# Performance work log

Measured on AMD Instinct MI355X. Metric: run time of the kernel, lower is better.

## Reference

```python
import jax, jax.numpy as jnp
import numpy as np

N = 50000   # nodes
E = 800000  # edges (avg degree 16)
H = 128     # hidden_dim / emb_dim
OUT = 128   # out_dim
NUM_BOND_TYPE = 6
NUM_BOND_DIR = 6


def setup_inputs() -> dict:
    key = jax.random.key(0)
    ks = jax.random.split(key, 12)
    s = 0.05
    return {
        "x": jax.random.normal(ks[0], (N, H), jnp.float32),
        "edge_index": jax.random.randint(ks[1], (2, E), 0, N),
        "edge_attr": jax.random.randint(ks[2], (E, 2), 0, 6),
        "prelu_a": jnp.float32(0.25),  # PReLU single shared slope (torch default)
        "W_enc": jax.random.normal(ks[3], (H, H), jnp.float32) * s,  # enc_to_dec, no bias
        "edge_emb1": jax.random.normal(ks[4], (NUM_BOND_TYPE, H), jnp.float32) * s,
        "edge_emb2": jax.random.normal(ks[5], (NUM_BOND_DIR, H), jnp.float32) * s,
        "W1": jax.random.normal(ks[6], (H, 2 * H), jnp.float32) * s,
        "b1": jnp.zeros((2 * H,), jnp.float32),
        "W2": jax.random.normal(ks[7], (2 * H, OUT), jnp.float32) * s,
        "b2": jnp.zeros((OUT,), jnp.float32),
    }


def reference(x, edge_index, edge_attr, prelu_a, W_enc, edge_emb1, edge_emb2, W1, b1, W2, b2):
    n = x.shape[0]
    # GNNDecoder: PReLU then enc_to_dec linear (no bias)
    x = jnp.where(x > 0, x, prelu_a * x)
    x = x @ W_enc

    # GINConv.forward: add self loops, self-loop edge_attr = [5, 0]
    loop = jnp.arange(n)
    src = jnp.concatenate([edge_index[0], loop])  # [E+N]
    dst = jnp.concatenate([edge_index[1], loop])  # [E+N]
    ea1 = jnp.concatenate([edge_attr[:, 0], jnp.full((n,), 5, edge_attr.dtype)])
    ea2 = jnp.concatenate([edge_attr[:, 1], jnp.zeros((n,), edge_attr.dtype)])

    # edge embedding lookup + gather-add message + scatter-add aggregate
    edge_emb = edge_emb1[ea1] + edge_emb2[ea2]          # [E+N, H]
    msg = x[src] + edge_emb                             # message(x_j, edge_attr)
    agg = jax.ops.segment_sum(msg, dst, num_segments=n)  # aggr='add'

    # update: MLP Linear(H,2H) -> SiLU -> Linear(2H,OUT)
    h = jax.nn.silu(agg @ W1 + b1)
    return h @ W2 + b2
```

## Files before the change

kernel.cpp:

```cpp
#include <hip/hip_runtime.h>

typedef unsigned short u16;
typedef unsigned int   u32;
typedef __attribute__((ext_vector_type(8))) short short8;
typedef __attribute__((ext_vector_type(4))) float f32x4;

__device__ __forceinline__ float bl(u32 u){ union{u32 i; float f;} c; c.i = u << 16; return c.f; }
__device__ __forceinline__ float bh(u32 u){ union{u32 i; float f;} c; c.i = u & 0xffff0000u; return c.f; }
__device__ __forceinline__ u16 f2b(float f){
  union{float f; u32 i;} c; c.f = f;
  return (u16)((c.i + 0x8000u) >> 16);
}
__device__ __forceinline__ u32 pk2(float a, float b){
  union{float f; u32 i;} x, y; x.f = a; y.f = b;
  return ((x.i + 0x8000u) >> 16) | ((y.i + 0x8000u) & 0xffff0000u);
}
__device__ __forceinline__ void accf(float* a, uint2 xq, float4 ef){
  a[0] += bl(xq.x) + ef.x;  a[1] += bh(xq.x) + ef.y;
  a[2] += bl(xq.y) + ef.z;  a[3] += bh(xq.y) + ef.w;
}

__device__ __forceinline__ void wave_scan_bsum(
    const int* __restrict__ bsum, int nb, int* __restrict__ sPre, int t)
{
  int carry = 0;
  for (int c0 = 0; c0 < nb; c0 += 64) {
    int idx = c0 + t;
    int b = (idx < nb) ? bsum[idx] : 0;
    int v = b;
    #pragma unroll
    for (int d = 1; d < 64; d <<= 1) {
      int u = __shfl_up(v, d);
      if (t >= d) v += u;
    }
    if (idx < nb) sPre[idx] = carry + v - b;
    carry += __shfl(v, 63);
  }
}

__global__ __launch_bounds__(256) void k_setup(
    const float* __restrict__ Wenc, const float* __restrict__ W1,
    const float* __restrict__ W2, const float* __restrict__ e1,
    const float* __restrict__ e2, u16* __restrict__ WencT,
    u16* __restrict__ W1T, u16* __restrict__ W2T,
    float* __restrict__ embF, int* __restrict__ cnt, int N)
{
  int i = blockIdx.x * 256 + threadIdx.x;
  if (i < 16384) {
    int n = i >> 7, k = i & 127;
    WencT[i] = f2b(Wenc[k * 128 + n]);
  } else if (i < 49152) {
    int j = i - 16384;
    int n = j >> 7, k = j & 127;
    W1T[j] = f2b(W1[k * 256 + n]);
  } else if (i < 81920) {
    int j = i - 49152;
    int n = j >> 8, k = j & 255;
    W2T[j] = f2b(W2[k * 128 + n]);
  } else if (i < 81920 + 4608) {
    int j = i - 81920;
    int comb = j >> 7, k = j & 127;
    int c1 = comb / 6, c2 = comb - c1 * 6;
    embF[j] = e1[c1 * 128 + k] + e2[c2 * 128 + k];
  } else {
    int j = i - 81920 - 4608;
    if (j < N) cnt[j] = 0;
  }
}

__global__ __launch_bounds__(256) void k_enc_count(
    const float* __restrict__ x, const float* __restrict__ pa,
    const u16* __restrict__ WT, u16* __restrict__ xenc, int N,
    const int* __restrict__ ei, int* __restrict__ cnt,
    int* __restrict__ rank, int E, int encBlocks)
{
  if ((int)blockIdx.x >= encBlocks) {
    int e = ((int)blockIdx.x - encBlocks) * 256 + threadIdx.x;
    if (e < E) rank[e] = atomicAdd(&cnt[ei[E + e]], 1);
    return;
  }

  const int K = 128, SK = 136, NT = 8;
  __shared__ u16 sB[128 * SK];

  const int t = threadIdx.x;
  #pragma unroll
  for (int j = 0; j < 8; j++) {
    int i = t + 256 * j;
    int n = i >> 4, k8 = i & 15;
    *(uint4*)&sB[n * SK + k8 * 8] = *(const uint4*)&WT[n * K + k8 * 8];
  }
  __syncthreads();

  const float slope = pa[0];
  const int lane = t & 63, wave = t >> 6, quad = lane >> 4, l16 = lane & 15;
  const int m0 = blockIdx.x * 128 + wave * 32;
  if (m0 >= N) return;

  f32x4 acc[2][NT];
  #pragma unroll
  for (int mr = 0; mr < 2; mr++)
    #pragma unroll
    for (int nt = 0; nt < NT; nt++) acc[mr][nt] = (f32x4){0.f, 0.f, 0.f, 0.f};

  #pragma unroll
  for (int ks = 0; ks < 4; ks++) {
    const int k0 = ks * 32 + quad * 8;
    union { u32 u[4]; short8 s; } a[2];
    #pragma unroll
    for (int mr = 0; mr < 2; mr++) {
      int row = m0 + mr * 16 + l16; row = min(row, N - 1);
      const float4* ap = (const float4*)&x[(size_t)row * 128 + k0];
      float4 f0 = ap[0], f1 = ap[1];
      float v0 = f0.x > 0.f ? f0.x : slope * f0.x;
      float v1 = f0.y > 0.f ? f0.y : slope * f0.y;
      float v2 = f0.z > 0.f ? f0.z : slope * f0.z;
      float v3 = f0.w > 0.f ? f0.w : slope * f0.w;
      float v4 = f1.x > 0.f ? f1.x : slope * f1.x;
      float v5 = f1.y > 0.f ? f1.y : slope * f1.y;
      float v6 = f1.z > 0.f ? f1.z : slope * f1.z;
      float v7 = f1.w > 0.f ? f1.w : slope * f1.w;
      a[mr].u[0] = pk2(v0, v1); a[mr].u[1] = pk2(v2, v3);
      a[mr].u[2] = pk2(v4, v5); a[mr].u[3] = pk2(v6, v7);
    }
    #pragma unroll
    for (int nt = 0; nt < NT; nt++) {
      short8 b = *(const short8*)&sB[(nt * 16 + l16) * SK + k0];
      acc[0][nt] = __builtin_amdgcn_mfma_f32_16x16x32_bf16(a[0].s, b, acc[0][nt], 0, 0, 0);
      acc[1][nt] = __builtin_amdgcn_mfma_f32_16x16x32_bf16(a[1].s, b, acc[1][nt], 0, 0, 0);
    }
  }

  #pragma unroll
  for (int mr = 0; mr < 2; mr++)
    #pragma unroll
    for (int nt = 0; nt < NT; nt++) {
      int col = nt * 16 + l16;
      #pragma unroll
      for (int r = 0; r < 4; r++) {
        int row = m0 + mr * 16 + quad * 4 + r;
        if (row < N) xenc[(size_t)row * 128 + col] = f2b(acc[mr][nt][r]);
      }
    }
}

__global__ __launch_bounds__(256) void k_scan_block(
    const int* __restrict__ cnt, int* __restrict__ offs,
    int* __restrict__ bsum, int n)
{
  __shared__ int sS[256];
  const int b = blockIdx.x, t = threadIdx.x;
  const int i0 = b * 1024 + t * 4;
  int4 v = make_int4(0, 0, 0, 0);
  if (i0 + 3 < n) v = *(const int4*)&cnt[i0];
  else {
    if (i0     < n) v.x = cnt[i0];
    if (i0 + 1 < n) v.y = cnt[i0 + 1];
    if (i0 + 2 < n) v.z = cnt[i0 + 2];
  }
  int s = v.x + v.y + v.z + v.w;
  sS[t] = s;
  __syncthreads();
  for (int d = 1; d < 256; d <<= 1) {
    int val = (t >= d) ? sS[t - d] : 0;
    __syncthreads();
    sS[t] += val;
    __syncthreads();
  }
  int ex = sS[t] - s;
  if (t == 255) bsum[b] = sS[t];
  int o0 = ex, o1 = o0 + v.x, o2 = o1 + v.y, o3 = o2 + v.z;
  if (i0     < n) offs[i0]     = o0;
  if (i0 + 1 < n) offs[i0 + 1] = o1;
  if (i0 + 2 < n) offs[i0 + 2] = o2;
  if (i0 + 3 < n) offs[i0 + 3] = o3;
}

__global__ __launch_bounds__(256) void k_fill(
    const int* __restrict__ ei, const int* __restrict__ ea,
    const int* __restrict__ offs, const int* __restrict__ rank,
    const int* __restrict__ bsum, int nb,
    u32* __restrict__ recs, int E)
{
  __shared__ int sPre[256];
  const int t = threadIdx.x;
  if (t < 64) wave_scan_bsum(bsum, nb, sPre, t);
  __syncthreads();

  int e = blockIdx.x * 256 + t;
  if (e >= E) return;
  int src = ei[e];
  int dst = ei[E + e];
  int2 a = *(const int2*)&ea[2 * e];
  int pos = offs[dst] + sPre[dst >> 10] + rank[e];
  recs[pos] = (u32)src | ((u32)(a.x * 6 + a.y) << 26);
}

__global__ __launch_bounds__(256) void k_gather(
    const int* __restrict__ offs, const int* __restrict__ bsum, int nb,
    const u32* __restrict__ recs, const float* __restrict__ embF,
    const u32* __restrict__ xenc32, u32* __restrict__ aggb, int N, int E)
{
  __shared__ float sE[36 * 128];
  __shared__ int sPre[256];

  const int t = threadIdx.x;
  for (int i = t; i < 1152; i += 256)
    ((float4*)sE)[i] = ((const float4*)embF)[i];
  if (t < 64) wave_scan_bsum(bsum, nb, sPre, t);
  __syncthreads();

  const int v = blockIdx.x * 4 + (t >> 6);
  if (v >= N) return;
  const int lane = t & 63, g = lane >> 5, sub = lane & 31;
  const u32 M = 0x3ffffffu;

  float a[4];
  #pragma unroll
  for (int j = 0; j < 4; j++) a[j] = 0.f;

  if (g == 0) {
    uint2 xq = *(const uint2*)&xenc32[(size_t)v * 64 + sub * 2];
    float4 eq = *(const float4*)&sE[30 * 128 + sub * 4];
    accf(a, xq, eq);
  }

  const int beg = offs[v] + sPre[v >> 10];
  const int end = (v == N - 1) ? E : (offs[v + 1] + sPre[(v + 1) >> 10]);

  for (int base = beg; base < end; base += 64) {
    u32 rv = 0;
    if (base + lane < end) rv = recs[base + lane];
    const int cnt = min(64, end - base);
    const int npair = cnt >> 1;
    int jj = 0;
    for (; jj + 8 <= npair; jj += 8) {
      u32 r0 = __shfl(rv, (jj + 0) * 2 + g);
      u32 r1 = __shfl(rv, (jj + 1) * 2 + g);
      u32 r2 = __shfl(rv, (jj + 2) * 2 + g);
      u32 r3 = __shfl(rv, (jj + 3) * 2 + g);
      u32 r4 = __shfl(rv, (jj + 4) * 2 + g);
      u32 r5 = __shfl(rv, (jj + 5) * 2 + g);
      u32 r6 = __shfl(rv, (jj + 6) * 2 + g);
      u32 r7 = __shfl(rv, (jj + 7) * 2 + g);
      uint2 x0 = *(const uint2*)&xenc32[(size_t)(r0 & M) * 64 + sub * 2];
      uint2 x1 = *(const uint2*)&xenc32[(size_t)(r1 & M) * 64 + sub * 2];
      uint2 x2 = *(const uint2*)&xenc32[(size_t)(r2 & M) * 64 + sub * 2];
      uint2 x3 = *(const uint2*)&xenc32[(size_t)(r3 & M) * 64 + sub * 2];
      uint2 x4 = *(const uint2*)&xenc32[(size_t)(r4 & M) * 64 + sub * 2];
      uint2 x5 = *(const uint2*)&xenc32[(size_t)(r5 & M) * 64 + sub * 2];
      uint2 x6 = *(const uint2*)&xenc32[(size_t)(r6 & M) * 64 + sub * 2];
      uint2 x7 = *(const uint2*)&xenc32[(size_t)(r7 & M) * 64 + sub * 2];
      float4 e0 = *(const float4*)&sE[(r0 >> 26) * 128 + sub * 4];
      float4 e1 = *(const float4*)&sE[(r1 >> 26) * 128 + sub * 4];
      float4 e2 = *(const float4*)&sE[(r2 >> 26) * 128 + sub * 4];
      float4 e3 = *(const float4*)&sE[(r3 >> 26) * 128 + sub * 4];
      float4 e4 = *(const float4*)&sE[(r4 >> 26) * 128 + sub * 4];
      float4 e5 = *(const float4*)&sE[(r5 >> 26) * 128 + sub * 4];
      float4 e6 = *(const float4*)&sE[(r6 >> 26) * 128 + sub * 4];
      float4 e7 = *(const float4*)&sE[(r7 >> 26) * 128 + sub * 4];
      accf(a, x0, e0); accf(a, x1, e1); accf(a, x2, e2); accf(a, x3, e3);
      accf(a, x4, e4); accf(a, x5, e5); accf(a, x6, e6); accf(a, x7, e7);
    }
    for (; jj < npair; jj++) {
      u32 r = __shfl(rv, jj * 2 + g);
      uint2 xq = *(const uint2*)&xenc32[(size_t)(r & M) * 64 + sub * 2];
      float4 eq = *(const float4*)&sE[(r >> 26) * 128 + sub * 4];
      accf(a, xq, eq);
    }
    if (cnt & 1) {
      u32 r = __shfl(rv, cnt - 1);
      if (g == 0) {
        uint2 xq = *(const uint2*)&xenc32[(size_t)(r & M) * 64 + sub * 2];
        float4 eq = *(const float4*)&sE[(r >> 26) * 128 + sub * 4];
        accf(a, xq, eq);
      }
    }
  }

  #pragma unroll
  for (int j = 0; j < 4; j++) a[j] += __shfl_xor(a[j], 32);

  if (g == 0) {
    uint2 o;
    o.x = pk2(a[0], a[1]);
    o.y = pk2(a[2], a[3]);
    *(uint2*)&aggb[(size_t)v * 64 + sub * 2] = o;
  }
}

__global__ __launch_bounds__(256) void k_mlp(
    const u16* __restrict__ aggb, const u16* __restrict__ W1T,
    const float* __restrict__ b1, const u16* __restrict__ W2T,
    const float* __restrict__ b2, float* __restrict__ out, int N)
{
  const int SK = 136;
  __shared__ u16 sW[128 * SK];
  __shared__ u16 sH[128 * SK];
  __shared__ float sB1[256];
  __shared__ float sB2[128];

  const int t = threadIdx.x;
  const int lane = t & 63, wave = t >> 6, quad = lane >> 4, l16 = lane & 15;
  const int m0 = blockIdx.x * 128 + wave * 32;

  if (t < 128) sB2[t] = b2[t];
  sB1[t] = b1[t];

  union { uint4 q; short8 s; } a[2][4];
  #pragma unroll
  for (int mr = 0; mr < 2; mr++) {
    int row = min(m0 + mr * 16 + l16, N - 1);
    #pragma unroll
    for (int ks = 0; ks < 4; ks++)
      a[mr][ks].q = *(const uint4*)&aggb[(size_t)row * 128 + ks * 32 + quad * 8];
  }

  f32x4 acc2[2][8];
  #pragma unroll
  for (int mr = 0; mr < 2; mr++)
    #pragma unroll
    for (int nt = 0; nt < 8; nt++) acc2[mr][nt] = (f32x4){0.f, 0.f, 0.f, 0.f};

  for (int half = 0; half < 2; half++) {
    #pragma unroll
    for (int j = 0; j < 8; j++) {
      int i = t + 256 * j;
      int n = i >> 4, k8 = i & 15;
      *(uint4*)&sW[n * SK + k8 * 8] =
          *(const uint4*)&W1T[(size_t)(half * 128 + n) * 128 + k8 * 8];
    }
    __syncthreads();

    f32x4 acc1[2][8];
    #pragma unroll
    for (int mr = 0; mr < 2; mr++)
      #pragma unroll
      for (int nt = 0; nt < 8; nt++) acc1[mr][nt] = (f32x4){0.f, 0.f, 0.f, 0.f};

    #pragma unroll
    for (int ks = 0; ks < 4; ks++) {
      const int k0 = ks * 32 + quad * 8;
      #pragma unroll
      for (int nt = 0; nt < 8; nt++) {
        short8 b = *(const short8*)&sW[(nt * 16 + l16) * SK + k0];
        acc1[0][nt] = __builtin_amdgcn_mfma_f32_16x16x32_bf16(a[0][ks].s, b, acc1[0][nt], 0, 0, 0);
        acc1[1][nt] = __builtin_amdgcn_mfma_f32_16x16x32_bf16(a[1][ks].s, b, acc1[1][nt], 0, 0, 0);
      }
    }

    #pragma unroll
    for (int mr = 0; mr < 2; mr++)
      #pragma unroll
      for (int nt = 0; nt < 8; nt++) {
        int col = nt * 16 + l16;
        float bias = sB1[half * 128 + col];
        #pragma unroll
        for (int r = 0; r < 4; r++) {
          float z = acc1[mr][nt][r] + bias;
          float s = z / (1.f + __expf(-z));
          sH[(wave * 32 + mr * 16 + quad * 4 + r) * SK + col] = f2b(s);
        }
      }
    __syncthreads();

    #pragma unroll
    for (int j = 0; j < 8; j++) {
      int i = t + 256 * j;
      int n = i >> 4, k8 = i & 15;
      *(uint4*)&sW[n * SK + k8 * 8] =
          *(const uint4*)&W2T[(size_t)n * 256 + half * 128 + k8 * 8];
    }
    __syncthreads();

    #pragma unroll
    for (int ks = 0; ks < 4; ks++) {
      const int k0 = ks * 32 + quad * 8;
      union { uint4 q; short8 s; } ah[2];
      #pragma unroll
      for (int mr = 0; mr < 2; mr++)
        ah[mr].q = *(const uint4*)&sH[(wave * 32 + mr * 16 + l16) * SK + k0];
      #pragma unroll
      for (int nt = 0; nt < 8; nt++) {
        short8 b = *(const short8*)&sW[(nt * 16 + l16) * SK + k0];
        acc2[0][nt] = __builtin_amdgcn_mfma_f32_16x16x32_bf16(ah[0].s, b, acc2[0][nt], 0, 0, 0);
        acc2[1][nt] = __builtin_amdgcn_mfma_f32_16x16x32_bf16(ah[1].s, b, acc2[1][nt], 0, 0, 0);
      }
    }
    __syncthreads();
  }

  #pragma unroll
  for (int mr = 0; mr < 2; mr++)
    #pragma unroll
    for (int nt = 0; nt < 8; nt++) {
      int col = nt * 16 + l16;
      float bias = sB2[col];
      #pragma unroll
      for (int r = 0; r < 4; r++) {
        int row = m0 + mr * 16 + quad * 4 + r;
        if (row < N) out[(size_t)row * 128 + col] = acc2[mr][nt][r] + bias;
      }
    }
}

extern "C" void kernel_launch(void* const* d_in, const int* in_sizes, int n_in,
                              void* d_out, int out_size, void* d_ws, size_t ws_size,
                              hipStream_t stream) {
  const float* x    = (const float*)d_in[0];
  const int*   ei   = (const int*)d_in[1];
  const int*   ea   = (const int*)d_in[2];
  const float* pa   = (const float*)d_in[3];
  const float* Wenc = (const float*)d_in[4];
  const float* e1   = (const float*)d_in[5];
  const float* e2   = (const float*)d_in[6];
  const float* W1   = (const float*)d_in[7];
  const float* b1   = (const float*)d_in[8];
  const float* W2   = (const float*)d_in[9];
  const float* b2   = (const float*)d_in[10];
  float* out = (float*)d_out;

  const int N = in_sizes[0] / 128;
  const int E = in_sizes[1] / 2;

  char* ws = (char*)d_ws;
  size_t off = 0;
  auto alloc = [&](size_t bytes) {
    void* p = ws + off;
    off = (off + bytes + 255) & ~(size_t)255;
    return p;
  };
  u16*   xenc   = (u16*)  alloc((size_t)N * 128 * 2);
  u32*   aggb   = (u32*)  alloc((size_t)N * 64 * 4);
  int*   cnt    = (int*)  alloc((size_t)N * 4);
  int*   offs   = (int*)  alloc((size_t)(N + 1) * 4);
  int*   rank   = (int*)  alloc((size_t)E * 4);
  int*   bsum   = (int*)  alloc(256 * 4);
  u32*   recs   = (u32*)  alloc((size_t)E * 4);
  u16*   WencT  = (u16*)  alloc(128 * 128 * 2);
  u16*   W1T    = (u16*)  alloc(256 * 128 * 2);
  u16*   W2T    = (u16*)  alloc(128 * 256 * 2);
  float* embF   = (float*)alloc(36 * 128 * 4);

  const int encBlocks   = (N + 127) / 128;
  const int edgeBlocks  = (E + 255) / 256;
  const int setupBlocks = (81920 + 4608 + N + 255) / 256;
  const int nb          = (N + 1023) / 1024;

  k_setup<<<setupBlocks, 256, 0, stream>>>(Wenc, W1, W2, e1, e2,
                                           WencT, W1T, W2T, embF, cnt, N);
  k_enc_count<<<encBlocks + edgeBlocks, 256, 0, stream>>>(
      x, pa, WencT, xenc, N, ei, cnt, rank, E, encBlocks);
  k_scan_block<<<nb, 256, 0, stream>>>(cnt, offs, bsum, N);
  k_fill<<<edgeBlocks, 256, 0, stream>>>(ei, ea, offs, rank, bsum, nb, recs, E);
  k_gather<<<(N + 3) / 4, 256, 0, stream>>>(
      offs, bsum, nb, recs, embF, (const u32*)xenc, aggb, N, E);
  k_mlp<<<encBlocks, 256, 0, stream>>>(
      (const u16*)aggb, W1T, b1, W2T, b2, out, N);
}
```

Before: 237.8 us.

## Split feature matrix into column-quarter planes and gather per quarter

Stores the encoded node features and the aggregate in four column-quarter planes (N x 32 bf16 each). The gather kernel now assigns 8 lanes per node, 8 nodes per wave, and loops over the four quarters so each quarter's working set is a quarter of the full table, aiming for better L2 locality in the random gathers. The embedding table in shared memory is also re-laid out per quarter. In exchange, each quarter pass rereads the edge records, and the 64-byte row pieces are narrower than the 256-byte rows gathered before.

```diff
diff --git a/kernel.cpp b/kernel.cpp
--- a/kernel.cpp
+++ b/kernel.cpp
@@ -14,10 +14,6 @@
 __device__ __forceinline__ u32 pk2(float a, float b){
   union{float f; u32 i;} x, y; x.f = a; y.f = b;
   return ((x.i + 0x8000u) >> 16) | ((y.i + 0x8000u) & 0xffff0000u);
-}
-__device__ __forceinline__ void accf(float* a, uint2 xq, float4 ef){
-  a[0] += bl(xq.x) + ef.x;  a[1] += bh(xq.x) + ef.y;
-  a[2] += bl(xq.y) + ef.z;  a[3] += bh(xq.y) + ef.w;
 }
 
 __device__ __forceinline__ void wave_scan_bsum(
@@ -70,7 +66,7 @@
 
 __global__ __launch_bounds__(256) void k_enc_count(
     const float* __restrict__ x, const float* __restrict__ pa,
-    const u16* __restrict__ WT, u16* __restrict__ xenc, int N,
+    const u16* __restrict__ WT, u16* __restrict__ xencQ, int N,
     const int* __restrict__ ei, int* __restrict__ cnt,
     int* __restrict__ rank, int E, int encBlocks)
 {
@@ -136,10 +132,12 @@
     #pragma unroll
     for (int nt = 0; nt < NT; nt++) {
       int col = nt * 16 + l16;
+      int q = col >> 5, cq = col & 31;
       #pragma unroll
       for (int r = 0; r < 4; r++) {
         int row = m0 + mr * 16 + quad * 4 + r;
-        if (row < N) xenc[(size_t)row * 128 + col] = f2b(acc[mr][nt][r]);
+        if (row < N)
+          xencQ[((size_t)q * N + row) * 32 + cq] = f2b(acc[mr][nt][r]);
       }
     }
 }
@@ -199,98 +197,69 @@
 __global__ __launch_bounds__(256) void k_gather(
     const int* __restrict__ offs, const int* __restrict__ bsum, int nb,
     const u32* __restrict__ recs, const float* __restrict__ embF,
-    const u32* __restrict__ xenc32, u32* __restrict__ aggb, int N, int E)
-{
-  __shared__ float sE[36 * 128];
+    const u32* __restrict__ xencQ, u32* __restrict__ aggbQ, int N, int E)
+{
+  const int ES = 36;
+  __shared__ float sE4[4 * 36 * ES];
   __shared__ int sPre[256];
 
   const int t = threadIdx.x;
-  for (int i = t; i < 1152; i += 256)
-    ((float4*)sE)[i] = ((const float4*)embF)[i];
+  for (int i = t; i < 4 * 36 * 8; i += 256) {
+    int q = i / (36 * 8);
+    int r = i - q * 36 * 8;
+    int c = r >> 3, s4 = r & 7;
+    float4 v = *(const float4*)&embF[c * 128 + q * 32 + s4 * 4];
+    *(float4*)&sE4[(q * 36 + c) * ES + s4 * 4] = v;
+  }
   if (t < 64) wave_scan_bsum(bsum, nb, sPre, t);
   __syncthreads();
 
-  const int v = blockIdx.x * 4 + (t >> 6);
-  if (v >= N) return;
-  const int lane = t & 63, g = lane >> 5, sub = lane & 31;
+  const int lane = t & 63, wave = t >> 6;
+  const int g = lane >> 3, sub = lane & 7;
+  const int v = blockIdx.x * 32 + wave * 8 + g;
+  const bool vok = v < N;
+  const int vc = vok ? v : N - 1;
+  const int beg = offs[vc] + sPre[vc >> 10];
+  const int end = (vc == N - 1) ? E : (offs[vc + 1] + sPre[(vc + 1) >> 10]);
+  const int deg = vok ? end - beg : 0;
   const u32 M = 0x3ffffffu;
 
-  float a[4];
-  #pragma unroll
-  for (int j = 0; j < 4; j++) a[j] = 0.f;
-
-  if (g == 0) {
-    uint2 xq = *(const uint2*)&xenc32[(size_t)v * 64 + sub * 2];
-    float4 eq = *(const float4*)&sE[30 * 128 + sub * 4];
-    accf(a, xq, eq);
-  }
-
-  const int beg = offs[v] + sPre[v >> 10];
-  const int end = (v == N - 1) ? E : (offs[v + 1] + sPre[(v + 1) >> 10]);
-
-  for (int base = beg; base < end; base += 64) {
-    u32 rv = 0;
-    if (base + lane < end) rv = recs[base + lane];
-    const int cnt = min(64, end - base);
-    const int npair = cnt >> 1;
-    int jj = 0;
-    for (; jj + 8 <= npair; jj += 8) {
-      u32 r0 = __shfl(rv, (jj + 0) * 2 + g);
-      u32 r1 = __shfl(rv, (jj + 1) * 2 + g);
-      u32 r2 = __shfl(rv, (jj + 2) * 2 + g);
-      u32 r3 = __shfl(rv, (jj + 3) * 2 + g);
-      u32 r4 = __shfl(rv, (jj + 4) * 2 + g);
-      u32 r5 = __shfl(rv, (jj + 5) * 2 + g);
-      u32 r6 = __shfl(rv, (jj + 6) * 2 + g);
-      u32 r7 = __shfl(rv, (jj + 7) * 2 + g);
-      uint2 x0 = *(const uint2*)&xenc32[(size_t)(r0 & M) * 64 + sub * 2];
-      uint2 x1 = *(const uint2*)&xenc32[(size_t)(r1 & M) * 64 + sub * 2];
-      uint2 x2 = *(const uint2*)&xenc32[(size_t)(r2 & M) * 64 + sub * 2];
-      uint2 x3 = *(const uint2*)&xenc32[(size_t)(r3 & M) * 64 + sub * 2];
-      uint2 x4 = *(const uint2*)&xenc32[(size_t)(r4 & M) * 64 + sub * 2];
-      uint2 x5 = *(const uint2*)&xenc32[(size_t)(r5 & M) * 64 + sub * 2];
-      uint2 x6 = *(const uint2*)&xenc32[(size_t)(r6 & M) * 64 + sub * 2];
-      uint2 x7 = *(const uint2*)&xenc32[(size_t)(r7 & M) * 64 + sub * 2];
-      float4 e0 = *(const float4*)&sE[(r0 >> 26) * 128 + sub * 4];
-      float4 e1 = *(const float4*)&sE[(r1 >> 26) * 128 + sub * 4];
-      float4 e2 = *(const float4*)&sE[(r2 >> 26) * 128 + sub * 4];
-      float4 e3 = *(const float4*)&sE[(r3 >> 26) * 128 + sub * 4];
-      float4 e4 = *(const float4*)&sE[(r4 >> 26) * 128 + sub * 4];
-      float4 e5 = *(const float4*)&sE[(r5 >> 26) * 128 + sub * 4];
-      float4 e6 = *(const float4*)&sE[(r6 >> 26) * 128 + sub * 4];
-      float4 e7 = *(const float4*)&sE[(r7 >> 26) * 128 + sub * 4];
-      accf(a, x0, e0); accf(a, x1, e1); accf(a, x2, e2); accf(a, x3, e3);
-      accf(a, x4, e4); accf(a, x5, e5); accf(a, x6, e6); accf(a, x7, e7);
-    }
-    for (; jj < npair; jj++) {
-      u32 r = __shfl(rv, jj * 2 + g);
-      uint2 xq = *(const uint2*)&xenc32[(size_t)(r & M) * 64 + sub * 2];
-      float4 eq = *(const float4*)&sE[(r >> 26) * 128 + sub * 4];
-      accf(a, xq, eq);
-    }
-    if (cnt & 1) {
-      u32 r = __shfl(rv, cnt - 1);
-      if (g == 0) {
-        uint2 xq = *(const uint2*)&xenc32[(size_t)(r & M) * 64 + sub * 2];
-        float4 eq = *(const float4*)&sE[(r >> 26) * 128 + sub * 4];
-        accf(a, xq, eq);
-      }
-    }
-  }
-
-  #pragma unroll
-  for (int j = 0; j < 4; j++) a[j] += __shfl_xor(a[j], 32);
-
-  if (g == 0) {
-    uint2 o;
-    o.x = pk2(a[0], a[1]);
-    o.y = pk2(a[2], a[3]);
-    *(uint2*)&aggb[(size_t)v * 64 + sub * 2] = o;
+  #pragma unroll
+  for (int q = 0; q < 4; q++) {
+    const u32* xq = xencQ + (size_t)q * N * 16;
+    const float* sEq = &sE4[q * 36 * ES];
+
+    uint2 xs = *(const uint2*)&xq[(size_t)vc * 16 + sub * 2];
+    float4 es = *(const float4*)&sEq[30 * ES + sub * 4];
+    float a0 = bl(xs.x) + es.x, a1 = bh(xs.x) + es.y;
+    float a2 = bl(xs.y) + es.z, a3 = bh(xs.y) + es.w;
+
+    for (int j0 = 0; j0 < deg; j0 += 8) {
+      int idx = beg + j0 + sub;
+      u32 rv = recs[min(idx, end - 1)];
+      #pragma unroll
+      for (int k = 0; k < 8; k++) {
+        u32 r = __shfl(rv, (lane & 56) + k);
+        if (j0 + k < deg) {
+          uint2 xr = *(const uint2*)&xq[(size_t)(r & M) * 16 + sub * 2];
+          float4 er = *(const float4*)&sEq[(r >> 26) * ES + sub * 4];
+          a0 += bl(xr.x) + er.x;  a1 += bh(xr.x) + er.y;
+          a2 += bl(xr.y) + er.z;  a3 += bh(xr.y) + er.w;
+        }
+      }
+    }
+
+    if (vok) {
+      uint2 o;
+      o.x = pk2(a0, a1);
+      o.y = pk2(a2, a3);
+      *(uint2*)&aggbQ[((size_t)q * N + vc) * 16 + sub * 2] = o;
+    }
   }
 }
 
 __global__ __launch_bounds__(256) void k_mlp(
-    const u16* __restrict__ aggb, const u16* __restrict__ W1T,
+    const u16* __restrict__ aggbQ, const u16* __restrict__ W1T,
     const float* __restrict__ b1, const u16* __restrict__ W2T,
     const float* __restrict__ b2, float* __restrict__ out, int N)
 {
@@ -313,7 +282,7 @@
     int row = min(m0 + mr * 16 + l16, N - 1);
     #pragma unroll
     for (int ks = 0; ks < 4; ks++)
-      a[mr][ks].q = *(const uint4*)&aggb[(size_t)row * 128 + ks * 32 + quad * 8];
+      a[mr][ks].q = *(const uint4*)&aggbQ[((size_t)ks * N + row) * 32 + quad * 8];
   }
 
   f32x4 acc2[2][8];
@@ -430,8 +399,8 @@
     off = (off + bytes + 255) & ~(size_t)255;
     return p;
   };
-  u16*   xenc   = (u16*)  alloc((size_t)N * 128 * 2);
-  u32*   aggb   = (u32*)  alloc((size_t)N * 64 * 4);
+  u16*   xencQ  = (u16*)  alloc((size_t)N * 128 * 2);
+  u32*   aggbQ  = (u32*)  alloc((size_t)N * 64 * 4);
   int*   cnt    = (int*)  alloc((size_t)N * 4);
   int*   offs   = (int*)  alloc((size_t)(N + 1) * 4);
   int*   rank   = (int*)  alloc((size_t)E * 4);
@@ -446,15 +415,16 @@
   const int edgeBlocks  = (E + 255) / 256;
   const int setupBlocks = (81920 + 4608 + N + 255) / 256;
   const int nb          = (N + 1023) / 1024;
+  const int gatherBlocks = (N + 31) / 32;
 
   k_setup<<<setupBlocks, 256, 0, stream>>>(Wenc, W1, W2, e1, e2,
                                            WencT, W1T, W2T, embF, cnt, N);
   k_enc_count<<<encBlocks + edgeBlocks, 256, 0, stream>>>(
-      x, pa, WencT, xenc, N, ei, cnt, rank, E, encBlocks);
+      x, pa, WencT, xencQ, N, ei, cnt, rank, E, encBlocks);
   k_scan_block<<<nb, 256, 0, stream>>>(cnt, offs, bsum, N);
   k_fill<<<edgeBlocks, 256, 0, stream>>>(ei, ea, offs, rank, bsum, nb, recs, E);
-  k_gather<<<(N + 3) / 4, 256, 0, stream>>>(
-      offs, bsum, nb, recs, embF, (const u32*)xenc, aggb, N, E);
+  k_gather<<<gatherBlocks, 256, 0, stream>>>(
+      offs, bsum, nb, recs, embF, (const u32*)xencQ, aggbQ, N, E);
   k_mlp<<<encBlocks, 256, 0, stream>>>(
-      (const u16*)aggb, W1T, b1, W2T, b2, out, N);
-}
+      (const u16*)aggbQ, W1T, b1, W2T, b2, out, N);
+}
```

Result: faster. 233.0 us (-2.0%).
